# Kernel optimization log

Measured on AMD Instinct MI355X. Metric: run time of the kernel, lower is better.

Reference implementation:

```python
import jax, jax.numpy as jnp
import numpy as np


def setup_inputs() -> dict:
    key = jax.random.key(0)
    k1, k2, k3 = jax.random.split(key, 3)
    B, S, C, D, V = 16, 2048, 16, 256, 100000
    value_seq = jax.random.randint(k1, (B, S, C), 0, V, dtype=jnp.int64)
    hidden = jax.random.normal(k2, (B, S, D), dtype=jnp.float32)
    value_table = jax.random.normal(k3, (V, D), dtype=jnp.float32)
    return {"value_seq": value_seq, "hidden": hidden, "value_table": value_table}


def reference(value_seq, hidden, value_table):
    # padding_idx=0: row 0 of the embedding table is zeros
    table = value_table.at[0].set(0.0)
    # gather: [B,S,C,D]
    value_embed = table[value_seq]
    # dot attention scores over the C context slots: [B,S,C]
    u = jnp.einsum('bsd,bscd->bsc', hidden, value_embed)
    p = jax.nn.softmax(u, axis=-1)
    # weighted combine: [B,S,D]
    o = jnp.einsum('bsc,bscd->bsd', p, value_embed)
    return o
```

## Files before the change

kernel.cpp:

```cpp
#include <hip/hip_runtime.h>


#define KV_C 16
#define KV_D 256
#define KV_TOKENS (16 * 2048)

__global__ __launch_bounds__(256) void kv_mem_kernel(
    const int* __restrict__ seq,
    const float* __restrict__ hidden,
    const float* __restrict__ table,
    float* __restrict__ out)
{
    const int wave = threadIdx.x >> 6;
    const int lane = threadIdx.x & 63;
    const int token = blockIdx.x * 4 + wave;

    const float4 h = *(const float4*)(hidden + (size_t)token * KV_D + lane * 4);

    const int* sp = seq + (size_t)token * KV_C;
    int myidx = (lane < KV_C) ? sp[lane] : 0;

    float4 e[KV_C];
    float  u[KV_C];

    #pragma unroll
    for (int c = 0; c < KV_C; ++c) {
        int idx = __shfl(myidx, c);
        float4 ev = make_float4(0.f, 0.f, 0.f, 0.f);
        if (idx != 0) {
            ev = *(const float4*)(table + (size_t)idx * KV_D + lane * 4);
        }
        e[c] = ev;
        u[c] = h.x * ev.x + h.y * ev.y + h.z * ev.z + h.w * ev.w;
    }

    #pragma unroll
    for (int s = 32; s >= 1; s >>= 1) {
        #pragma unroll
        for (int c = 0; c < KV_C; ++c) {
            u[c] += __shfl_xor(u[c], s);
        }
    }

    float m = u[0];
    #pragma unroll
    for (int c = 1; c < KV_C; ++c) m = fmaxf(m, u[c]);
    float sum = 0.f;
    #pragma unroll
    for (int c = 0; c < KV_C; ++c) {
        u[c] = __expf(u[c] - m);
        sum += u[c];
    }
    const float inv = 1.0f / sum;

    float4 o = make_float4(0.f, 0.f, 0.f, 0.f);
    #pragma unroll
    for (int c = 0; c < KV_C; ++c) {
        const float w = u[c] * inv;
        o.x += w * e[c].x;
        o.y += w * e[c].y;
        o.z += w * e[c].z;
        o.w += w * e[c].w;
    }

    *(float4*)(out + (size_t)token * KV_D + lane * 4) = o;
}

extern "C" void kernel_launch(void* const* d_in, const int* in_sizes, int n_in,
                              void* d_out, int out_size, void* d_ws, size_t ws_size,
                              hipStream_t stream) {
    const int*   seq    = (const int*)d_in[0];
    const float* hidden = (const float*)d_in[1];
    const float* table  = (const float*)d_in[2];
    float*       out    = (float*)d_out;

    dim3 grid(KV_TOKENS / 4);
    dim3 block(256);
    kv_mem_kernel<<<grid, block, 0, stream>>>(seq, hidden, table, out);
}
```

Before: 228.2 us.

## Chunk context slots with online softmax and branchless masked gathers

New measurement: 228.1 us. No clear change (-0.0%).

```diff
diff --git a/kernel.cpp b/kernel.cpp
--- a/kernel.cpp
+++ b/kernel.cpp
@@ -3,9 +3,10 @@
 
 #define KV_C 16
 #define KV_D 256
+#define KV_CHUNK 8
 #define KV_TOKENS (16 * 2048)
 
-__global__ __launch_bounds__(256) void kv_mem_kernel(
+__global__ __launch_bounds__(256, 4) void kv_mem_kernel(
     const int* __restrict__ seq,
     const float* __restrict__ hidden,
     const float* __restrict__ table,
@@ -19,49 +20,61 @@
 
     const int* sp = seq + (size_t)token * KV_C;
     int myidx = (lane < KV_C) ? sp[lane] : 0;
+    const unsigned long long nz = __ballot(myidx != 0);
 
-    float4 e[KV_C];
-    float  u[KV_C];
+    float m_run = 0.0f;
+    float l_run = 0.0f;
+    float4 o = make_float4(0.f, 0.f, 0.f, 0.f);
 
     #pragma unroll
-    for (int c = 0; c < KV_C; ++c) {
-        int idx = __shfl(myidx, c);
-        float4 ev = make_float4(0.f, 0.f, 0.f, 0.f);
-        if (idx != 0) {
-            ev = *(const float4*)(table + (size_t)idx * KV_D + lane * 4);
+    for (int ch = 0; ch < KV_C / KV_CHUNK; ++ch) {
+        const int cbase = ch * KV_CHUNK;
+
+        float4 e[KV_CHUNK];
+        #pragma unroll
+        for (int j = 0; j < KV_CHUNK; ++j) {
+            const int idx = __shfl(myidx, cbase + j);
+            e[j] = *(const float4*)(table + (size_t)idx * KV_D + lane * 4);
         }
-        e[c] = ev;
-        u[c] = h.x * ev.x + h.y * ev.y + h.z * ev.z + h.w * ev.w;
+
+        float u[KV_CHUNK];
+        #pragma unroll
+        for (int j = 0; j < KV_CHUNK; ++j) {
+            const float msk = ((nz >> (cbase + j)) & 1ULL) ? 1.0f : 0.0f;
+            u[j] = msk * (h.x * e[j].x + h.y * e[j].y +
+                          h.z * e[j].z + h.w * e[j].w);
+        }
+
+        #pragma unroll
+        for (int s = 32; s >= 1; s >>= 1) {
+            #pragma unroll
+            for (int j = 0; j < KV_CHUNK; ++j) {
+                u[j] += __shfl_xor(u[j], s);
+            }
+        }
+
+        float m_new = m_run;
+        #pragma unroll
+        for (int j = 0; j < KV_CHUNK; ++j) m_new = fmaxf(m_new, u[j]);
+        const float scale = __expf(m_run - m_new);
+        l_run *= scale;
+        o.x *= scale; o.y *= scale; o.z *= scale; o.w *= scale;
+        #pragma unroll
+        for (int j = 0; j < KV_CHUNK; ++j) {
+            const float w = __expf(u[j] - m_new);
+            l_run += w;
+            const float msk = ((nz >> (cbase + j)) & 1ULL) ? 1.0f : 0.0f;
+            const float wm = w * msk;
+            o.x += wm * e[j].x;
+            o.y += wm * e[j].y;
+            o.z += wm * e[j].z;
+            o.w += wm * e[j].w;
+        }
+        m_run = m_new;
     }
 
-    #pragma unroll
-    for (int s = 32; s >= 1; s >>= 1) {
-        #pragma unroll
-        for (int c = 0; c < KV_C; ++c) {
-            u[c] += __shfl_xor(u[c], s);
-        }
-    }
-
-    float m = u[0];
-    #pragma unroll
-    for (int c = 1; c < KV_C; ++c) m = fmaxf(m, u[c]);
-    float sum = 0.f;
-    #pragma unroll
-    for (int c = 0; c < KV_C; ++c) {
-        u[c] = __expf(u[c] - m);
-        sum += u[c];
-    }
-    const float inv = 1.0f / sum;
-
-    float4 o = make_float4(0.f, 0.f, 0.f, 0.f);
-    #pragma unroll
-    for (int c = 0; c < KV_C; ++c) {
-        const float w = u[c] * inv;
-        o.x += w * e[c].x;
-        o.y += w * e[c].y;
-        o.z += w * e[c].z;
-        o.w += w * e[c].w;
-    }
+    const float inv = 1.0f / l_run;
+    o.x *= inv; o.y *= inv; o.z *= inv; o.w *= inv;
 
     *(float4*)(out + (size_t)token * KV_D + lane * 4) = o;
 }
```
